# Optimization experiments

Hardware: AMD Instinct MI355X
Metric: run time of the kernel (lower is better)

The kernel has to match this reference:

```python
import jax, jax.numpy as jnp
import numpy as np

K = 3
STRIDE = 1
PAD = 1
DIL = 1


def _unfold(a):
    # a: (N, C, H, W) -> patches (N, C, K*K, oH, oW), matching torch.F.unfold
    # channel-major ordering (c slowest, then kernel row, then kernel col).
    N, C, H, W = a.shape
    oH = (H + 2 * PAD - DIL * (K - 1) - 1) // STRIDE + 1
    oW = (W + 2 * PAD - DIL * (K - 1) - 1) // STRIDE + 1
    ap = jnp.pad(a, ((0, 0), (0, 0), (PAD, PAD), (PAD, PAD)))
    cols = []
    for i in range(K):
        for j in range(K):
            cols.append(ap[:, :,
                           i * DIL: i * DIL + (oH - 1) * STRIDE + 1: STRIDE,
                           j * DIL: j * DIL + (oW - 1) * STRIDE + 1: STRIDE])
    return jnp.stack(cols, axis=2)  # (N, C, K*K, oH, oW)


def setup_inputs() -> dict:
    key = jax.random.key(0)
    k1, k2, k3, k4, k5 = jax.random.split(key, 5)
    N, C, O, H, W = 4, 128, 256, 128, 128
    x = jax.random.normal(k1, (N, C, H, W), dtype=jnp.float32)
    depth = jax.random.uniform(k2, (N, 1, H, W), dtype=jnp.float32)
    camera_params = jax.random.normal(k3, (N, 4), dtype=jnp.float32)
    weight = jax.random.normal(k4, (O, C, K, K), dtype=jnp.float32) * 0.05
    bias = jax.random.normal(k5, (O,), dtype=jnp.float32) * 0.05
    return {"x": x, "depth": depth, "camera_params": camera_params,
            "weight": weight, "bias": bias}


def reference(x, depth, camera_params, weight, bias):
    # camera_params is accepted but unused, mirroring the torch module.
    O, C = weight.shape[0], weight.shape[1]
    xp = _unfold(x)        # (N, C, kk, oH, oW)
    dp = _unfold(depth)    # (N, 1, kk, oH, oW)
    w = weight.reshape(O, C, K * K)
    # depth-modulated im2col GEMM: sum_{c,p} w[o,c,p] * x_patch * d_patch
    out = jnp.einsum('ocp,ncpxy->noxy', w, xp * dp)
    return out + bias[None, :, None, None]
```

## Files before the change

### kernel.cpp

```cpp
#include <hip/hip_runtime.h>
#include <stdint.h>


#define C_IN 128
#define O_OUT 256
#define HW 128
#define NB 4
#define PADW 130

#define XD_ELEMS ((size_t)NB * PADW * PADW * C_IN)
#define XD_BYTES (XD_ELEMS * 2)
#define WT_ELEMS ((size_t)O_OUT * C_IN * 9)
#define WT_BYTES (WT_ELEMS * 2)

typedef __attribute__((ext_vector_type(8))) short short8;
typedef __attribute__((ext_vector_type(4))) float f32x4;
typedef __attribute__((ext_vector_type(2))) float f32x2;
typedef __attribute__((ext_vector_type(4))) unsigned uint4v;

__device__ __forceinline__ unsigned f2bf_bits(float f) {
  unsigned u = __builtin_bit_cast(unsigned, f);
  return (u + 0x7fffu + ((u >> 16) & 1u)) >> 16;
}

__device__ __forceinline__ void async_load16(const void* g, void* l) {
  __builtin_amdgcn_global_load_lds(
      (__attribute__((address_space(1))) void*)g,
      (__attribute__((address_space(3))) void*)l, 16, 0, 0);
}

__global__ __launch_bounds__(256) void prep_all(const float* __restrict__ x,
                                                const float* __restrict__ depth,
                                                const float* __restrict__ w,
                                                short* __restrict__ xd,
                                                short* __restrict__ wt2) {
  const int R = blockIdx.x;

  if (R >= NB * HW + NB) {
    int gid = (R - (NB * HW + NB)) * 4608 + threadIdx.x;
#pragma unroll
    for (int i = 0; i < 18; ++i, gid += 256) {
      const int j = gid & 7;
      const int t = (gid >> 3) & 3;
      const int lane = (gid >> 5) & 63;
      const int wm = (gid >> 11) & 1;
      const int g2 = gid >> 12;
      const int s = g2 % 36;
      const int o0 = g2 / 36;
      const int ln = lane & 15, q = lane >> 4;
      const int o = (o0 << 7) + (wm << 6) + (t << 4) + ln;
      const int cc = s / 9;
      const int tap = s % 9;
      const int c = (cc << 5) + (q << 3) + j;
      wt2[gid] = (short)f2bf_bits(w[((size_t)o * C_IN + c) * 9 + tap]);
    }
    return;
  }

  if (R >= NB * HW) {
    const int n = R - NB * HW;
    uint4v* base0 = (uint4v*)(xd + (size_t)n * PADW * PADW * C_IN);
    uint4v* base1 = (uint4v*)(xd + ((size_t)n * PADW + (PADW - 1)) * PADW * C_IN);
    const uint4v z = {0u, 0u, 0u, 0u};
    const int per_row = PADW * C_IN * 2 / 16;
    for (int i = threadIdx.x; i < per_row; i += 256) {
      base0[i] = z;
      base1[i] = z;
    }
    return;
  }

  __shared__ short s[C_IN * PADW];

  const int n = R >> 7, y = R & 127;
  const int tid = threadIdx.x;
  const int lane = tid & 63;
  const int wave = tid >> 6;

  {
    unsigned* row = (unsigned*)(xd + ((size_t)(n * PADW + y + 1) * PADW) * C_IN);
    if (tid < 64) row[tid] = 0u;
    else if (tid < 128) row[(size_t)(PADW - 1) * 64 + (tid - 64)] = 0u;
  }

  const f32x2 d2 = *(const f32x2*)(depth + ((size_t)n * HW + y) * HW + 2 * lane);
  const float* xrow = x + (((size_t)n * C_IN) * HW + y) * HW + 2 * lane;
  unsigned* s32 = (unsigned*)s;
#pragma unroll 8
  for (int ci = 0; ci < 32; ++ci) {
    const int c = ci * 4 + wave;
    const f32x2 v = *(const f32x2*)(xrow + (size_t)c * HW * HW);
    s32[c * 65 + lane] = f2bf_bits(v.x * d2.x) | (f2bf_bits(v.y * d2.y) << 16);
  }
  __syncthreads();

  const unsigned short* s16 = (const unsigned short*)s;
  unsigned* orow = (unsigned*)(xd + ((size_t)(n * PADW + y + 1) * PADW + 1) * C_IN);
#pragma unroll 8
  for (int i = 0; i < 32; ++i) {
    const int flat = tid + i * 256;
    const int px = flat >> 6, cp = flat & 63;
    const unsigned lo = s16[(2 * cp) * PADW + px];
    const unsigned hi = s16[(2 * cp + 1) * PADW + px];
    orow[flat] = lo | (hi << 16);
  }
}

__global__ __launch_bounds__(256, 2) void conv_mfma(
    const short* __restrict__ xd, const short* __restrict__ wt2,
    const float* __restrict__ bias, float* __restrict__ out) {
  __shared__ short xbuf[16640];

  const int tid = threadIdx.x;
  const int bx = blockIdx.x;
  const int n = bx >> 6;
  const int y = (bx & 63) << 1;
  const int o0b = blockIdx.y;
  const int lane = tid & 63;
  const int wave = tid >> 6;
  const int wm = wave & 1, wn = wave >> 1;
  const int ln = lane & 15, q = lane >> 4;

  const short* wbase =
      wt2 + (size_t)o0b * 147456 + (wm << 11) + (lane << 5);

  const short* xsrc0 = xd + (size_t)(n * PADW + y) * PADW * C_IN +
                       (tid >> 2) * C_IN + (tid & 3) * 8;
  short* xdst0 = xbuf + tid * 8;

  f32x4 acc[4][8] = {};
  short8 areg[2][4];

  auto loadA = [&](int s, int p) {
#pragma unroll
    for (int t = 0; t < 4; ++t)
      areg[p][t] = *(const short8*)(wbase + (size_t)s * 4096 + t * 8);
  };
  auto stageX = [&](int cc) {
    const short* sp = xsrc0 + (cc << 5);
#pragma unroll
    for (int j = 0; j < 8; ++j)
      async_load16(sp + j * 8192, xdst0 + j * 2048);
    if (tid < 32) async_load16(sp + 8 * 8192, xdst0 + 8 * 2048);
  };

  loadA(0, 0);
  stageX(0);
  __syncthreads();

#pragma unroll
  for (int cc = 0; cc < 4; ++cc) {
#pragma unroll
    for (int tap = 0; tap < 9; ++tap) {
      const int s = cc * 9 + tap;
      if (s + 1 < 36) loadA(s + 1, (s + 1) & 1);

      const int ti = tap / 3, tj = tap % 3;
      const int rbase = (wn + ti) * 130 + tj;

      short8 b[8];
#pragma unroll
      for (int u = 0; u < 8; ++u)
        b[u] = *(const short8*)(xbuf + (rbase + (u << 4) + ln) * 32 + (q << 3));
#pragma unroll
      for (int t = 0; t < 4; ++t)
#pragma unroll
        for (int u = 0; u < 8; ++u)
          acc[t][u] = __builtin_amdgcn_mfma_f32_16x16x32_bf16(
              areg[s & 1][t], b[u], acc[t][u], 0, 0, 0);
    }
    if (cc + 1 < 4) {
      __syncthreads();
      stageX(cc + 1);
      __syncthreads();
    }
  }

#pragma unroll
  for (int t = 0; t < 4; ++t) {
    const int ob = (o0b << 7) + (wm << 6) + (t << 4) + (q << 2);
#pragma unroll
    for (int u = 0; u < 8; ++u) {
      const int xcol = (u << 4) + ln;
      const int yrow = y + wn;
#pragma unroll
      for (int r = 0; r < 4; ++r) {
        const int o = ob + r;
        out[(((size_t)n * O_OUT + o) * HW + yrow) * HW + xcol] =
            acc[t][u][r] + bias[o];
      }
    }
  }
}

__global__ void conv_naive(const float* __restrict__ x,
                           const float* __restrict__ depth,
                           const float* __restrict__ w,
                           const float* __restrict__ bias,
                           float* __restrict__ out) {
  const int gid = blockIdx.x * 256 + threadIdx.x;
  if (gid >= NB * O_OUT * HW * HW) return;
  const int xc = gid & 127;
  const int y = (gid >> 7) & 127;
  const int o = (gid >> 14) & 255;
  const int n = gid >> 22;
  float s = bias[o];
  for (int c = 0; c < C_IN; ++c)
    for (int i = 0; i < 3; ++i) {
      const int yy = y + i - 1;
      if (yy < 0 || yy >= HW) continue;
      for (int j = 0; j < 3; ++j) {
        const int xx = xc + j - 1;
        if (xx < 0 || xx >= HW) continue;
        s += w[((o * C_IN + c) * 3 + i) * 3 + j] *
             x[(((size_t)n * C_IN + c) * HW + yy) * HW + xx] *
             depth[((size_t)n * HW + yy) * HW + xx];
      }
    }
  out[gid] = s;
}

extern "C" void kernel_launch(void* const* d_in, const int* in_sizes, int n_in,
                              void* d_out, int out_size, void* d_ws, size_t ws_size,
                              hipStream_t stream) {
  const float* x = (const float*)d_in[0];
  const float* depth = (const float*)d_in[1];
  const float* weight = (const float*)d_in[3];
  const float* bias = (const float*)d_in[4];
  float* out = (float*)d_out;

  const size_t need = XD_BYTES + WT_BYTES;
  if (ws_size < need) {
    conv_naive<<<(NB * O_OUT * HW * HW + 255) / 256, 256, 0, stream>>>(
        x, depth, weight, bias, out);
    return;
  }

  short* xd = (short*)d_ws;
  short* wt2 = (short*)((char*)d_ws + XD_BYTES);

  prep_all<<<NB * HW + NB + 64, 256, 0, stream>>>(x, depth, weight, xd, wt2);
  conv_mfma<<<dim3(NB * HW / 2, 2), 256, 0, stream>>>(xd, wt2, bias, out);
}
```

Baseline: 135.5 us.

## Double-buffer input staging in conv, split prep rows, and coalesce weight layout

The conv kernel now double-buffers the input channel chunk in LDS and spreads the async loads for the next chunk across the tap loop, which removes the two barriers and exposed load latency between chunks. MFMA sections are bracketed with setprio. The prep kernel splits each row into two channel halves, giving twice as many blocks, and writes 16-byte vectors from a padded LDS transpose. The weight repack layout changes so that each lane's A-fragment loads are contiguous across lanes. Doubling the LDS buffer raises per-block shared memory, which may reduce occupancy.

```diff
diff --git a/kernel.cpp b/kernel.cpp
--- a/kernel.cpp
+++ b/kernel.cpp
@@ -35,14 +35,15 @@
                                                 short* __restrict__ xd,
                                                 short* __restrict__ wt2) {
   const int R = blockIdx.x;
-
-  if (R >= NB * HW + NB) {
-    int gid = (R - (NB * HW + NB)) * 4608 + threadIdx.x;
+  const int tid = threadIdx.x;
+
+  if (R >= NB * HW * 2 + NB) {
+    int gid = (R - (NB * HW * 2 + NB)) * 4608 + tid;
 #pragma unroll
     for (int i = 0; i < 18; ++i, gid += 256) {
       const int j = gid & 7;
-      const int t = (gid >> 3) & 3;
-      const int lane = (gid >> 5) & 63;
+      const int lane = (gid >> 3) & 63;
+      const int t = (gid >> 9) & 3;
       const int wm = (gid >> 11) & 1;
       const int g2 = gid >> 12;
       const int s = g2 % 36;
@@ -57,59 +58,62 @@
     return;
   }
 
-  if (R >= NB * HW) {
-    const int n = R - NB * HW;
+  if (R >= NB * HW * 2) {
+    const int n = R - NB * HW * 2;
     uint4v* base0 = (uint4v*)(xd + (size_t)n * PADW * PADW * C_IN);
     uint4v* base1 = (uint4v*)(xd + ((size_t)n * PADW + (PADW - 1)) * PADW * C_IN);
     const uint4v z = {0u, 0u, 0u, 0u};
     const int per_row = PADW * C_IN * 2 / 16;
-    for (int i = threadIdx.x; i < per_row; i += 256) {
+    for (int i = tid; i < per_row; i += 256) {
       base0[i] = z;
       base1[i] = z;
     }
     return;
   }
 
-  __shared__ short s[C_IN * PADW];
-
-  const int n = R >> 7, y = R & 127;
-  const int tid = threadIdx.x;
+  __shared__ __align__(16) unsigned s32[HW * 36];
+
+  const int n = R >> 8;
+  const int y = (R >> 1) & 127;
+  const int h = R & 1;
   const int lane = tid & 63;
   const int wave = tid >> 6;
 
   {
-    unsigned* row = (unsigned*)(xd + ((size_t)(n * PADW + y + 1) * PADW) * C_IN);
-    if (tid < 64) row[tid] = 0u;
-    else if (tid < 128) row[(size_t)(PADW - 1) * 64 + (tid - 64)] = 0u;
+    unsigned* row = (unsigned*)(xd + (size_t)(n * PADW + y + 1) * PADW * C_IN);
+    if (tid < 32) row[(h << 5) + tid] = 0u;
+    else if (tid < 64) row[(size_t)(PADW - 1) * 64 + (h << 5) + (tid - 32)] = 0u;
   }
 
   const f32x2 d2 = *(const f32x2*)(depth + ((size_t)n * HW + y) * HW + 2 * lane);
-  const float* xrow = x + (((size_t)n * C_IN) * HW + y) * HW + 2 * lane;
-  unsigned* s32 = (unsigned*)s;
-#pragma unroll 8
-  for (int ci = 0; ci < 32; ++ci) {
-    const int c = ci * 4 + wave;
-    const f32x2 v = *(const f32x2*)(xrow + (size_t)c * HW * HW);
-    s32[c * 65 + lane] = f2bf_bits(v.x * d2.x) | (f2bf_bits(v.y * d2.y) << 16);
+  const float* xrow =
+      x + (((size_t)(n * C_IN + (h << 6)) * HW) + y) * HW + 2 * lane;
+#pragma unroll
+  for (int it = 0; it < 8; ++it) {
+    const int cp = (wave << 3) + it;
+    const f32x2 va = *(const f32x2*)(xrow + (size_t)(2 * cp) * HW * HW);
+    const f32x2 vb = *(const f32x2*)(xrow + (size_t)(2 * cp + 1) * HW * HW);
+    s32[(2 * lane) * 36 + cp] =
+        f2bf_bits(va.x * d2.x) | (f2bf_bits(vb.x * d2.x) << 16);
+    s32[(2 * lane + 1) * 36 + cp] =
+        f2bf_bits(va.y * d2.y) | (f2bf_bits(vb.y * d2.y) << 16);
   }
   __syncthreads();
 
-  const unsigned short* s16 = (const unsigned short*)s;
   unsigned* orow = (unsigned*)(xd + ((size_t)(n * PADW + y + 1) * PADW + 1) * C_IN);
-#pragma unroll 8
-  for (int i = 0; i < 32; ++i) {
-    const int flat = tid + i * 256;
-    const int px = flat >> 6, cp = flat & 63;
-    const unsigned lo = s16[(2 * cp) * PADW + px];
-    const unsigned hi = s16[(2 * cp + 1) * PADW + px];
-    orow[flat] = lo | (hi << 16);
+#pragma unroll
+  for (int i = 0; i < 4; ++i) {
+    const int flat = tid + (i << 8);
+    const int px = flat >> 3, jj = flat & 7;
+    const uint4v v = *(const uint4v*)&s32[px * 36 + (jj << 2)];
+    *(uint4v*)&orow[(size_t)px * 64 + (h << 5) + (jj << 2)] = v;
   }
 }
 
 __global__ __launch_bounds__(256, 2) void conv_mfma(
     const short* __restrict__ xd, const short* __restrict__ wt2,
     const float* __restrict__ bias, float* __restrict__ out) {
-  __shared__ short xbuf[16640];
+  __shared__ __align__(16) short xbuf[2][16640];
 
   const int tid = threadIdx.x;
   const int bx = blockIdx.x;
@@ -121,12 +125,10 @@
   const int wm = wave & 1, wn = wave >> 1;
   const int ln = lane & 15, q = lane >> 4;
 
-  const short* wbase =
-      wt2 + (size_t)o0b * 147456 + (wm << 11) + (lane << 5);
+  const short* wbase = wt2 + (size_t)o0b * 147456 + (wm << 11) + (lane << 3);
 
   const short* xsrc0 = xd + (size_t)(n * PADW + y) * PADW * C_IN +
                        (tid >> 2) * C_IN + (tid & 3) * 8;
-  short* xdst0 = xbuf + tid * 8;
 
   f32x4 acc[4][8] = {};
   short8 areg[2][4];
@@ -134,18 +136,17 @@
   auto loadA = [&](int s, int p) {
 #pragma unroll
     for (int t = 0; t < 4; ++t)
-      areg[p][t] = *(const short8*)(wbase + (size_t)s * 4096 + t * 8);
+      areg[p][t] = *(const short8*)(wbase + (size_t)s * 4096 + t * 512);
   };
-  auto stageX = [&](int cc) {
-    const short* sp = xsrc0 + (cc << 5);
+
+  {
+    short* xdst = &xbuf[0][0] + tid * 8;
 #pragma unroll
     for (int j = 0; j < 8; ++j)
-      async_load16(sp + j * 8192, xdst0 + j * 2048);
-    if (tid < 32) async_load16(sp + 8 * 8192, xdst0 + 8 * 2048);
-  };
-
+      async_load16(xsrc0 + j * 8192, xdst + j * 2048);
+    if (tid < 32) async_load16(xsrc0 + 8 * 8192, xdst + 8 * 2048);
+  }
   loadA(0, 0);
-  stageX(0);
   __syncthreads();
 
 #pragma unroll
@@ -155,25 +156,32 @@
       const int s = cc * 9 + tap;
       if (s + 1 < 36) loadA(s + 1, (s + 1) & 1);
 
+      if (cc + 1 < 4) {
+        const short* sp = xsrc0 + ((cc + 1) << 5);
+        short* xdst = &xbuf[(cc + 1) & 1][0] + tid * 8;
+        if (tap < 8) async_load16(sp + tap * 8192, xdst + tap * 2048);
+        if (tap == 0 && tid < 32)
+          async_load16(sp + 8 * 8192, xdst + 8 * 2048);
+      }
+
       const int ti = tap / 3, tj = tap % 3;
       const int rbase = (wn + ti) * 130 + tj;
 
       short8 b[8];
 #pragma unroll
       for (int u = 0; u < 8; ++u)
-        b[u] = *(const short8*)(xbuf + (rbase + (u << 4) + ln) * 32 + (q << 3));
+        b[u] = *(const short8*)(&xbuf[cc & 1][0] +
+                                (rbase + (u << 4) + ln) * 32 + (q << 3));
+      __builtin_amdgcn_s_setprio(1);
 #pragma unroll
       for (int t = 0; t < 4; ++t)
 #pragma unroll
         for (int u = 0; u < 8; ++u)
           acc[t][u] = __builtin_amdgcn_mfma_f32_16x16x32_bf16(
               areg[s & 1][t], b[u], acc[t][u], 0, 0, 0);
-    }
-    if (cc + 1 < 4) {
-      __syncthreads();
-      stageX(cc + 1);
-      __syncthreads();
-    }
+      __builtin_amdgcn_s_setprio(0);
+    }
+    if (cc + 1 < 4) __syncthreads();
   }
 
 #pragma unroll
@@ -239,6 +247,6 @@
   short* xd = (short*)d_ws;
   short* wt2 = (short*)((char*)d_ws + XD_BYTES);
 
-  prep_all<<<NB * HW + NB + 64, 256, 0, stream>>>(x, depth, weight, xd, wt2);
+  prep_all<<<NB * HW * 2 + NB + 64, 256, 0, stream>>>(x, depth, weight, xd, wt2);
   conv_mfma<<<dim3(NB * HW / 2, 2), 256, 0, stream>>>(xd, wt2, bias, out);
 }
```

New measurement: 128.4 us. 1.06x faster.

## Double-buffer input tile in LDS with swizzle and interleaved async staging

Applied to the files above, without the earlier changes.

The conv kernel's LDS input tile is now double-buffered. The next channel chunk is staged with async global-to-LDS loads spread across the tap loop, replacing the two barriers around a bulk stage. The LDS layout is XOR-swizzled to cut bank conflicts on the B-fragment reads. The weight prep layout changes so each lane's A-fragment loads are contiguous per tile, and setprio raises priority around the MFMA block. LDS use doubles to about 66KB per block, which may limit the two-blocks-per-CU occupancy target.

```diff
diff --git a/kernel.cpp b/kernel.cpp
--- a/kernel.cpp
+++ b/kernel.cpp
@@ -35,20 +35,20 @@
                                                 short* __restrict__ xd,
                                                 short* __restrict__ wt2) {
   const int R = blockIdx.x;
+  const int tid = threadIdx.x;
 
   if (R >= NB * HW + NB) {
-    int gid = (R - (NB * HW + NB)) * 4608 + threadIdx.x;
+    int gid = (R - (NB * HW + NB)) * 4608 + tid;
 #pragma unroll
     for (int i = 0; i < 18; ++i, gid += 256) {
       const int j = gid & 7;
-      const int t = (gid >> 3) & 3;
-      const int lane = (gid >> 5) & 63;
-      const int wm = (gid >> 11) & 1;
+      const int lane = (gid >> 3) & 63;
+      const int T = (gid >> 9) & 7;
       const int g2 = gid >> 12;
       const int s = g2 % 36;
       const int o0 = g2 / 36;
       const int ln = lane & 15, q = lane >> 4;
-      const int o = (o0 << 7) + (wm << 6) + (t << 4) + ln;
+      const int o = (o0 << 7) + (T << 4) + ln;
       const int cc = s / 9;
       const int tap = s % 9;
       const int c = (cc << 5) + (q << 3) + j;
@@ -63,7 +63,7 @@
     uint4v* base1 = (uint4v*)(xd + ((size_t)n * PADW + (PADW - 1)) * PADW * C_IN);
     const uint4v z = {0u, 0u, 0u, 0u};
     const int per_row = PADW * C_IN * 2 / 16;
-    for (int i = threadIdx.x; i < per_row; i += 256) {
+    for (int i = tid; i < per_row; i += 256) {
       base0[i] = z;
       base1[i] = z;
     }
@@ -73,7 +73,6 @@
   __shared__ short s[C_IN * PADW];
 
   const int n = R >> 7, y = R & 127;
-  const int tid = threadIdx.x;
   const int lane = tid & 63;
   const int wave = tid >> 6;
 
@@ -109,7 +108,7 @@
 __global__ __launch_bounds__(256, 2) void conv_mfma(
     const short* __restrict__ xd, const short* __restrict__ wt2,
     const float* __restrict__ bias, float* __restrict__ out) {
-  __shared__ short xbuf[16640];
+  __shared__ __align__(16) short xbuf[2][16640];
 
   const int tid = threadIdx.x;
   const int bx = blockIdx.x;
@@ -121,12 +120,10 @@
   const int wm = wave & 1, wn = wave >> 1;
   const int ln = lane & 15, q = lane >> 4;
 
-  const short* wbase =
-      wt2 + (size_t)o0b * 147456 + (wm << 11) + (lane << 5);
+  const short* wbase = wt2 + (size_t)o0b * 147456 + (wm << 11) + (lane << 3);
 
   const short* xsrc0 = xd + (size_t)(n * PADW + y) * PADW * C_IN +
-                       (tid >> 2) * C_IN + (tid & 3) * 8;
-  short* xdst0 = xbuf + tid * 8;
+                       (tid >> 2) * C_IN + ((tid & 3) ^ ((tid >> 3) & 3)) * 8;
 
   f32x4 acc[4][8] = {};
   short8 areg[2][4];
@@ -134,18 +131,17 @@
   auto loadA = [&](int s, int p) {
 #pragma unroll
     for (int t = 0; t < 4; ++t)
-      areg[p][t] = *(const short8*)(wbase + (size_t)s * 4096 + t * 8);
+      areg[p][t] = *(const short8*)(wbase + (size_t)s * 4096 + t * 512);
   };
-  auto stageX = [&](int cc) {
-    const short* sp = xsrc0 + (cc << 5);
+
+  {
+    short* xdst = &xbuf[0][0] + tid * 8;
 #pragma unroll
     for (int j = 0; j < 8; ++j)
-      async_load16(sp + j * 8192, xdst0 + j * 2048);
-    if (tid < 32) async_load16(sp + 8 * 8192, xdst0 + 8 * 2048);
-  };
-
+      async_load16(xsrc0 + j * 8192, xdst + j * 2048);
+    if (tid < 32) async_load16(xsrc0 + 8 * 8192, xdst + 8 * 2048);
+  }
   loadA(0, 0);
-  stageX(0);
   __syncthreads();
 
 #pragma unroll
@@ -155,34 +151,43 @@
       const int s = cc * 9 + tap;
       if (s + 1 < 36) loadA(s + 1, (s + 1) & 1);
 
+      if (cc + 1 < 4) {
+        const short* sp = xsrc0 + ((cc + 1) << 5);
+        short* xdst = &xbuf[(cc + 1) & 1][0] + tid * 8;
+        if (tap < 8) async_load16(sp + tap * 8192, xdst + tap * 2048);
+        if (tap == 0 && tid < 32)
+          async_load16(sp + 8 * 8192, xdst + 8 * 2048);
+      }
+
       const int ti = tap / 3, tj = tap % 3;
       const int rbase = (wn + ti) * 130 + tj;
 
       short8 b[8];
 #pragma unroll
-      for (int u = 0; u < 8; ++u)
-        b[u] = *(const short8*)(xbuf + (rbase + (u << 4) + ln) * 32 + (q << 3));
+      for (int u = 0; u < 8; ++u) {
+        const int px = rbase + (u << 4) + ln;
+        const int qx = (q ^ ((px >> 1) & 3)) << 3;
+        b[u] = *(const short8*)(&xbuf[cc & 1][0] + px * 32 + qx);
+      }
+      __builtin_amdgcn_s_setprio(1);
 #pragma unroll
       for (int t = 0; t < 4; ++t)
 #pragma unroll
         for (int u = 0; u < 8; ++u)
           acc[t][u] = __builtin_amdgcn_mfma_f32_16x16x32_bf16(
               areg[s & 1][t], b[u], acc[t][u], 0, 0, 0);
-    }
-    if (cc + 1 < 4) {
-      __syncthreads();
-      stageX(cc + 1);
-      __syncthreads();
-    }
-  }
-
+      __builtin_amdgcn_s_setprio(0);
+    }
+    if (cc + 1 < 4) __syncthreads();
+  }
+
+  const int yrow = y + wn;
 #pragma unroll
   for (int t = 0; t < 4; ++t) {
     const int ob = (o0b << 7) + (wm << 6) + (t << 4) + (q << 2);
 #pragma unroll
     for (int u = 0; u < 8; ++u) {
       const int xcol = (u << 4) + ln;
-      const int yrow = y + wn;
 #pragma unroll
       for (int r = 0; r < 4; ++r) {
         const int o = ob + r;
```

Measured after the change: 132.8 us. -2.0%, faster.
